# Kernel optimization log

Hardware: AMD Instinct MI355X
Metric: run time of the kernel (lower is better)

The kernel has to match this reference:

```python
import jax, jax.numpy as jnp
import numpy as np

N = 128
HID = 512
NUM_IRREPS = 7

_ISO = np.array([
    [1,0,1,0,0,0,0],
    [0,1,0,1,1,0,0],
    [1,0,1,0,0,0,0],
    [0,1,0,1,1,0,0],
    [0,1,0,1,1,0,0],
    [0,0,0,0,0,1,0],
    [0,0,0,0,0,0,1],
], dtype=np.float32)


def setup_inputs() -> dict:
    key = jax.random.key(0)
    k1, k2 = jax.random.split(key)
    x = jax.random.normal(k1, (2, N, N, HID), dtype=jnp.float32)
    # xavier_uniform with relu gain on [num_irreps, num_irreps]
    gain = float(np.sqrt(2.0))
    bound = gain * float(np.sqrt(6.0 / (NUM_IRREPS + NUM_IRREPS)))
    weight = jax.random.uniform(k2, (NUM_IRREPS, NUM_IRREPS), dtype=jnp.float32,
                                minval=-bound, maxval=bound)
    iso_matrix = jnp.asarray(_ISO)
    return {"x": x, "weight": weight, "iso_matrix": iso_matrix}


def _decompose(M):
    # M: [h, n, n] -> [7, h, n, n], isotypic components under S_n conjugation.
    n = M.shape[-1]
    eye = jnp.eye(n, dtype=M.dtype)
    off = 1.0 - eye
    d = jnp.diagonal(M, axis1=-2, axis2=-1)                 # [h, n]
    dbar = jnp.mean(d, axis=-1, keepdims=True)              # [h, 1]
    P1 = dbar[..., None] * eye                              # diag mean (trivial)
    P2 = (d - dbar)[..., None] * eye                        # diag deviation (standard)
    O = M * off                                             # off-diagonal part
    s = jnp.sum(O, axis=(-2, -1)) / (n * (n - 1))           # [h]
    P3 = s[..., None, None] * off                           # offdiag mean (trivial)
    Op = O - P3
    r = jnp.sum(Op, axis=-1)                                # row sums, [h, n]
    c = jnp.sum(Op, axis=-2)                                # col sums, [h, n]
    xr = ((n - 1) * r + c) / (n * (n - 2))
    yc = ((n - 1) * c + r) / (n * (n - 2))
    P4 = xr[..., :, None] * off                             # row standard copy
    P5 = yc[..., None, :] * off                             # col standard copy
    R = Op - P4 - P5                                        # zero diag / row / col sums
    Rt = jnp.swapaxes(R, -1, -2)
    P6 = 0.5 * (R + Rt)                                     # irrep (n-2,2)
    P7 = 0.5 * (R - Rt)                                     # irrep (n-2,1,1)
    return jnp.stack([P1, P2, P3, P4, P5, P6, P7])          # [7, h, n, n]


def reference(x, weight, iso_matrix):
    # x: [2, n, n, hidden] -> transpose(1,3): [2, hidden, n, n]
    xt = jnp.transpose(x, (0, 3, 2, 1))
    A, B = xt[0], xt[1]                                     # [h, n, n]
    params = weight * iso_matrix                            # [7, 7]
    a = _decompose(A)                                       # [7, h, n, n]
    b = _decompose(B)
    # params @ comps, then sum over output irrep axis (fused into one einsum)
    A_out = jnp.einsum('ij,jhmn->hmn', params, a)
    B_out = jnp.einsum('ij,jhmn->hmn', params, b)
    out = jnp.stack([A_out, B_out])                         # [2, h, n, n]
    return jnp.transpose(out, (0, 3, 2, 1))                 # [2, n, n, hidden]
```

## Files before the change

kernel.cpp:

```cpp
#include <hip/hip_runtime.h>
#include <math.h>

#define N 128
#define HID 512
#define NH (N * HID)
#define SNH ((size_t)N * NH)
#define NPAIRS (N * (N + 1) / 2)

#define OFF_SA 0
#define OFF_SB 131072
#define OFF_DG 262144
#define OFF_XR 393216
#define OFF_YC 524288
#define OFF_SV 655360
#define OFF_DB 656384

typedef float vf4 __attribute__((ext_vector_type(4)));
union F4 { vf4 v; float f[4]; };

__global__ __launch_bounds__(512)
void schur_reduce(const float* __restrict__ x,
                  float* __restrict__ Sa, float* __restrict__ Sb,
                  float* __restrict__ Dg) {
    const int blk = blockIdx.x;
    const int s   = blk >> 7;
    const int idx = blk & 127;
    const int tid = threadIdx.x;
    const int ht  = tid & 127;
    const int q   = tid >> 7;
    const int hoff = ht * 4;

    const float* xs   = x + (size_t)s * SNH;
    const float* xrow = xs + (size_t)idx * NH;

    F4 sa; sa.v = (vf4)(0.f);
    for (int a = q; a < N; a += 4) {
        F4 v; v.v = *reinterpret_cast<const vf4*>(xs + (size_t)a * NH + idx * HID + hoff);
        #pragma unroll
        for (int j = 0; j < 4; ++j) sa.f[j] += v.f[j];
    }
    F4 sb; sb.v = (vf4)(0.f);
    for (int b = q; b < N; b += 4) {
        F4 v; v.v = *reinterpret_cast<const vf4*>(xrow + b * HID + hoff);
        #pragma unroll
        for (int j = 0; j < 4; ++j) sb.f[j] += v.f[j];
    }

    __shared__ F4 red[4][128];
    red[q][ht] = sa;
    __syncthreads();
    if (q == 0) {
        F4 t;
        #pragma unroll
        for (int j = 0; j < 4; ++j)
            t.f[j] = red[0][ht].f[j] + red[1][ht].f[j] + red[2][ht].f[j] + red[3][ht].f[j];
        *reinterpret_cast<vf4*>(Sa + ((size_t)s * N + idx) * HID + hoff) = t.v;
    }
    __syncthreads();
    red[q][ht] = sb;
    __syncthreads();
    if (q == 0) {
        F4 t;
        #pragma unroll
        for (int j = 0; j < 4; ++j)
            t.f[j] = red[0][ht].f[j] + red[1][ht].f[j] + red[2][ht].f[j] + red[3][ht].f[j];
        *reinterpret_cast<vf4*>(Sb + ((size_t)s * N + idx) * HID + hoff) = t.v;
        const vf4 dv = *reinterpret_cast<const vf4*>(xrow + idx * HID + hoff);
        *reinterpret_cast<vf4*>(Dg + ((size_t)s * N + idx) * HID + hoff) = dv;
    }
}

__global__ __launch_bounds__(512)
void schur_stats(const float* __restrict__ Sa, const float* __restrict__ Sb,
                 const float* __restrict__ Dg,
                 float* __restrict__ Xr, float* __restrict__ Yc,
                 float* __restrict__ Sv, float* __restrict__ Db) {
    const int blk = blockIdx.x;
    const int s   = blk >> 4;
    const int hc  = blk & 15;
    const int t   = threadIdx.x;
    const int iq  = t >> 5;
    const int hl  = t & 31;
    const int h   = hc * 32 + hl;
    const size_t base = (size_t)s * N * HID;

    float T = 0.f, D = 0.f;
    #pragma unroll
    for (int i = iq; i < N; i += 16) {
        T += Sa[base + (size_t)i * HID + h];
        D += Dg[base + (size_t)i * HID + h];
    }

    __shared__ float redT[16][32];
    __shared__ float redD[16][32];
    __shared__ float shS[32];
    redT[iq][hl] = T;
    redD[iq][hl] = D;
    __syncthreads();
    if (iq == 0) {
        float Tt = 0.f, Dd = 0.f;
        #pragma unroll
        for (int q = 0; q < 16; ++q) { Tt += redT[q][hl]; Dd += redD[q][hl]; }
        const float sh   = (Tt - Dd) * (1.0f / 16256.0f);
        const float dbar = Dd * (1.0f / 128.0f);
        Sv[s * HID + h] = sh;
        Db[s * HID + h] = dbar;
        shS[hl] = sh;
    }
    __syncthreads();

    const float sh    = shS[hl];
    const float k127s = 127.0f * sh;
    const float inv   = 1.0f / 16128.0f;
    #pragma unroll
    for (int i = iq; i < N; i += 16) {
        const size_t o = base + (size_t)i * HID + h;
        const float d = Dg[o];
        const float r = Sa[o] - d - k127s;
        const float c = Sb[o] - d - k127s;
        Xr[o] = (127.0f * r + c) * inv;
        Yc[o] = (127.0f * c + r) * inv;
    }
}

__global__ __launch_bounds__(256)
void schur_out(const float* __restrict__ x, const float* __restrict__ w,
               const float* __restrict__ iso,
               const float* __restrict__ Xr, const float* __restrict__ Yc,
               const float* __restrict__ Sv, const float* __restrict__ Db,
               float* __restrict__ out) {
    const int t  = threadIdx.x;
    const int k  = t >> 7;
    const int ht = t & 127;
    const int hoff = ht * 4;

    float c[7];
    #pragma unroll
    for (int j = 0; j < 7; ++j) {
        float acc = 0.f;
        #pragma unroll
        for (int i = 0; i < 7; ++i) acc += w[i * 7 + j] * iso[i * 7 + j];
        c[j] = acc;
    }
    const float c1 = c[0], c2 = c[1], c3 = c[2], c4 = c[3], c5 = c[4];
    const float al = 0.5f * (c[5] + c[6]);
    const float be = 0.5f * (c[5] - c[6]);

    const int pg0 = blockIdx.x * 8;

    #define TRI_OFF(aa) ((aa) * N - (((aa) * ((aa) - 1)) >> 1))
    #pragma unroll
    for (int it = 0; it < 4; ++it) {
        const int pg = pg0 + it * 2 + k;
        const int s  = (pg >= NPAIRS) ? 1 : 0;
        const int p  = pg - s * NPAIRS;

        int a = (int)((257.0f - sqrtf((float)(66049 - 8 * p))) * 0.5f);
        if (a < 0) a = 0;
        if (a > N - 1) a = N - 1;
        while (a > 0 && TRI_OFF(a) > p) --a;
        while (TRI_OFF(a + 1) <= p) ++a;
        const int b = a + (p - TRI_OFF(a));

        const size_t sbase    = (size_t)s * SNH;
        const size_t statbase = (size_t)s * N * HID;

        if (a == b) {
            F4 v;  v.v  = *reinterpret_cast<const vf4*>(x + sbase + ((size_t)a * N + a) * HID + hoff);
            F4 db; db.v = *reinterpret_cast<const vf4*>(Db + (size_t)s * HID + hoff);
            F4 o;
            #pragma unroll
            for (int j = 0; j < 4; ++j)
                o.f[j] = c1 * db.f[j] + c2 * (v.f[j] - db.f[j]);
            __builtin_nontemporal_store(o.v,
                reinterpret_cast<vf4*>(out + sbase + ((size_t)a * N + a) * HID + hoff));
            continue;
        }

        F4 va;  va.v  = *reinterpret_cast<const vf4*>(x + sbase + ((size_t)a * N + b) * HID + hoff);
        F4 vb;  vb.v  = *reinterpret_cast<const vf4*>(x + sbase + ((size_t)b * N + a) * HID + hoff);
        F4 xra; xra.v = *reinterpret_cast<const vf4*>(Xr + statbase + (size_t)a * HID + hoff);
        F4 xrb; xrb.v = *reinterpret_cast<const vf4*>(Xr + statbase + (size_t)b * HID + hoff);
        F4 yca; yca.v = *reinterpret_cast<const vf4*>(Yc + statbase + (size_t)a * HID + hoff);
        F4 ycb; ycb.v = *reinterpret_cast<const vf4*>(Yc + statbase + (size_t)b * HID + hoff);
        F4 sh;  sh.v  = *reinterpret_cast<const vf4*>(Sv + (size_t)s * HID + hoff);

        F4 oab, oba;
        #pragma unroll
        for (int j = 0; j < 4; ++j) {
            const float U = va.f[j] - sh.f[j] - xrb.f[j] - yca.f[j];
            const float V = vb.f[j] - sh.f[j] - xra.f[j] - ycb.f[j];
            oab.f[j] = c3 * sh.f[j] + c4 * xrb.f[j] + c5 * yca.f[j] + al * U + be * V;
            oba.f[j] = c3 * sh.f[j] + c4 * xra.f[j] + c5 * ycb.f[j] + al * V + be * U;
        }
        __builtin_nontemporal_store(oab.v,
            reinterpret_cast<vf4*>(out + sbase + ((size_t)a * N + b) * HID + hoff));
        __builtin_nontemporal_store(oba.v,
            reinterpret_cast<vf4*>(out + sbase + ((size_t)b * N + a) * HID + hoff));
    }
}

extern "C" void kernel_launch(void* const* d_in, const int* in_sizes, int n_in,
                              void* d_out, int out_size, void* d_ws, size_t ws_size,
                              hipStream_t stream) {
    const float* x   = (const float*)d_in[0];
    const float* w   = (const float*)d_in[1];
    const float* iso = (const float*)d_in[2];
    float* out = (float*)d_out;
    float* ws  = (float*)d_ws;

    float* Sa = ws + OFF_SA;
    float* Sb = ws + OFF_SB;
    float* Dg = ws + OFF_DG;
    float* Xr = ws + OFF_XR;
    float* Yc = ws + OFF_YC;
    float* Sv = ws + OFF_SV;
    float* Db = ws + OFF_DB;

    schur_reduce<<<2 * N, 512, 0, stream>>>(x, Sa, Sb, Dg);
    schur_stats<<<32, 512, 0, stream>>>(Sa, Sb, Dg, Xr, Yc, Sv, Db);
    schur_out<<<(2 * NPAIRS) / 8, 256, 0, stream>>>(x, w, iso, Xr, Yc, Sv, Db, out);
}
```

Measured before the change: 54.58 us.

## Fuse row and column reductions into single tiled pass over x

Replaces the reduce kernel, which read x twice (once for column sums, once for row sums), with a tiled kernel that reads each 8x8 tile of x once. From that single read it produces per-tile row and column partial sums and the diagonal. The stats kernel then sums the 16 partials per index. This halves the main read traffic of the reduction phase, at the cost of larger partial-sum buffers and more work in the low-parallelism stats kernel.

```diff
diff --git a/kernel.cpp b/kernel.cpp
--- a/kernel.cpp
+++ b/kernel.cpp
@@ -7,71 +7,75 @@
 #define SNH ((size_t)N * NH)
 #define NPAIRS (N * (N + 1) / 2)
 
-#define OFF_SA 0
-#define OFF_SB 131072
-#define OFF_DG 262144
-#define OFF_XR 393216
-#define OFF_YC 524288
-#define OFF_SV 655360
-#define OFF_DB 656384
+#define OFF_PSR 0
+#define OFF_PSC 2097152
+#define OFF_DG  4194304
+#define OFF_XR  4325376
+#define OFF_YC  4456448
+#define OFF_SV  4587520
+#define OFF_DB  4588544
 
 typedef float vf4 __attribute__((ext_vector_type(4)));
 union F4 { vf4 v; float f[4]; };
 
 __global__ __launch_bounds__(512)
-void schur_reduce(const float* __restrict__ x,
-                  float* __restrict__ Sa, float* __restrict__ Sb,
-                  float* __restrict__ Dg) {
-    const int blk = blockIdx.x;
-    const int s   = blk >> 7;
-    const int idx = blk & 127;
+void schur_tile(const float* __restrict__ x,
+                float* __restrict__ PSrow, float* __restrict__ PScol,
+                float* __restrict__ Dg) {
+    const int bi = blockIdx.x;
+    const int s  = bi >> 8;
+    const int ar = (bi >> 4) & 15;
+    const int br = bi & 15;
     const int tid = threadIdx.x;
-    const int ht  = tid & 127;
-    const int q   = tid >> 7;
-    const int hoff = ht * 4;
-
-    const float* xs   = x + (size_t)s * SNH;
-    const float* xrow = xs + (size_t)idx * NH;
-
-    F4 sa; sa.v = (vf4)(0.f);
-    for (int a = q; a < N; a += 4) {
-        F4 v; v.v = *reinterpret_cast<const vf4*>(xs + (size_t)a * NH + idx * HID + hoff);
-        #pragma unroll
-        for (int j = 0; j < 4; ++j) sa.f[j] += v.f[j];
-    }
-    F4 sb; sb.v = (vf4)(0.f);
-    for (int b = q; b < N; b += 4) {
-        F4 v; v.v = *reinterpret_cast<const vf4*>(xrow + b * HID + hoff);
-        #pragma unroll
-        for (int j = 0; j < 4; ++j) sb.f[j] += v.f[j];
-    }
-
-    __shared__ F4 red[4][128];
-    red[q][ht] = sa;
+    const int hg  = tid & 127;
+    const int qd  = tid >> 7;
+    const int hoff = hg * 4;
+    const bool diag = (ar == br);
+
+    const float* tbase = x + (size_t)s * SNH + (size_t)(ar * 8) * NH
+                           + (br * 8) * HID + hoff;
+
+    F4 colacc[8];
+    #pragma unroll
+    for (int b = 0; b < 8; ++b) colacc[b].v = (vf4)(0.f);
+
+    __shared__ F4 red[4][8][128];
+
+    #pragma unroll
+    for (int ra = 0; ra < 2; ++ra) {
+        const int al = qd * 2 + ra;
+        const float* rp = tbase + (size_t)al * NH;
+        F4 rowacc; rowacc.v = (vf4)(0.f);
+        F4 dgv;    dgv.v    = (vf4)(0.f);
+        #pragma unroll
+        for (int b = 0; b < 8; ++b) {
+            F4 v; v.v = *reinterpret_cast<const vf4*>(rp + b * HID);
+            rowacc.v += v.v;
+            colacc[b].v += v.v;
+            if (diag && b == al) dgv = v;
+        }
+        const int a = ar * 8 + al;
+        *reinterpret_cast<vf4*>(PSrow + (((size_t)(s * 16 + br) * 128 + a) * 512 + hoff)) = rowacc.v;
+        if (diag)
+            *reinterpret_cast<vf4*>(Dg + (((size_t)s * 128 + a) * 512 + hoff)) = dgv.v;
+    }
+
+    #pragma unroll
+    for (int b = 0; b < 8; ++b) red[qd][b][hg] = colacc[b];
     __syncthreads();
-    if (q == 0) {
+
+    #pragma unroll
+    for (int k = 0; k < 2; ++k) {
+        const int b = qd * 2 + k;
         F4 t;
-        #pragma unroll
-        for (int j = 0; j < 4; ++j)
-            t.f[j] = red[0][ht].f[j] + red[1][ht].f[j] + red[2][ht].f[j] + red[3][ht].f[j];
-        *reinterpret_cast<vf4*>(Sa + ((size_t)s * N + idx) * HID + hoff) = t.v;
-    }
-    __syncthreads();
-    red[q][ht] = sb;
-    __syncthreads();
-    if (q == 0) {
-        F4 t;
-        #pragma unroll
-        for (int j = 0; j < 4; ++j)
-            t.f[j] = red[0][ht].f[j] + red[1][ht].f[j] + red[2][ht].f[j] + red[3][ht].f[j];
-        *reinterpret_cast<vf4*>(Sb + ((size_t)s * N + idx) * HID + hoff) = t.v;
-        const vf4 dv = *reinterpret_cast<const vf4*>(xrow + idx * HID + hoff);
-        *reinterpret_cast<vf4*>(Dg + ((size_t)s * N + idx) * HID + hoff) = dv;
+        t.v = (red[0][b][hg].v + red[1][b][hg].v) + (red[2][b][hg].v + red[3][b][hg].v);
+        const int gb = br * 8 + b;
+        *reinterpret_cast<vf4*>(PScol + (((size_t)(s * 16 + ar) * 128 + gb) * 512 + hoff)) = t.v;
     }
 }
 
 __global__ __launch_bounds__(512)
-void schur_stats(const float* __restrict__ Sa, const float* __restrict__ Sb,
+void schur_stats(const float* __restrict__ PSrow, const float* __restrict__ PScol,
                  const float* __restrict__ Dg,
                  float* __restrict__ Xr, float* __restrict__ Yc,
                  float* __restrict__ Sv, float* __restrict__ Db) {
@@ -82,13 +86,21 @@
     const int iq  = t >> 5;
     const int hl  = t & 31;
     const int h   = hc * 32 + hl;
-    const size_t base = (size_t)s * N * HID;
-
+
+    float sa8[8], sb8[8], d8[8];
     float T = 0.f, D = 0.f;
     #pragma unroll
-    for (int i = iq; i < N; i += 16) {
-        T += Sa[base + (size_t)i * HID + h];
-        D += Dg[base + (size_t)i * HID + h];
+    for (int k = 0; k < 8; ++k) {
+        const int i = iq + k * 16;
+        float sa = 0.f, sb = 0.f;
+        #pragma unroll
+        for (int tt = 0; tt < 16; ++tt) {
+            sa += PScol[((size_t)(s * 16 + tt) * 128 + i) * 512 + h];
+            sb += PSrow[((size_t)(s * 16 + tt) * 128 + i) * 512 + h];
+        }
+        const float d = Dg[((size_t)s * 128 + i) * 512 + h];
+        sa8[k] = sa; sb8[k] = sb; d8[k] = d;
+        T += sa; D += d;
     }
 
     __shared__ float redT[16][32];
@@ -112,14 +124,15 @@
     const float sh    = shS[hl];
     const float k127s = 127.0f * sh;
     const float inv   = 1.0f / 16128.0f;
-    #pragma unroll
-    for (int i = iq; i < N; i += 16) {
-        const size_t o = base + (size_t)i * HID + h;
-        const float d = Dg[o];
-        const float r = Sa[o] - d - k127s;
-        const float c = Sb[o] - d - k127s;
-        Xr[o] = (127.0f * r + c) * inv;
-        Yc[o] = (127.0f * c + r) * inv;
+    const size_t base = (size_t)s * N * HID;
+    #pragma unroll
+    for (int k = 0; k < 8; ++k) {
+        const int i = iq + k * 16;
+        const float d = d8[k];
+        const float r = sa8[k] - d - k127s;
+        const float c = sb8[k] - d - k127s;
+        Xr[base + (size_t)i * HID + h] = (127.0f * r + c) * inv;
+        Yc[base + (size_t)i * HID + h] = (127.0f * c + r) * inv;
     }
 }
 
@@ -209,15 +222,15 @@
     float* out = (float*)d_out;
     float* ws  = (float*)d_ws;
 
-    float* Sa = ws + OFF_SA;
-    float* Sb = ws + OFF_SB;
-    float* Dg = ws + OFF_DG;
-    float* Xr = ws + OFF_XR;
-    float* Yc = ws + OFF_YC;
-    float* Sv = ws + OFF_SV;
-    float* Db = ws + OFF_DB;
-
-    schur_reduce<<<2 * N, 512, 0, stream>>>(x, Sa, Sb, Dg);
-    schur_stats<<<32, 512, 0, stream>>>(Sa, Sb, Dg, Xr, Yc, Sv, Db);
+    float* PSrow = ws + OFF_PSR;
+    float* PScol = ws + OFF_PSC;
+    float* Dg    = ws + OFF_DG;
+    float* Xr    = ws + OFF_XR;
+    float* Yc    = ws + OFF_YC;
+    float* Sv    = ws + OFF_SV;
+    float* Db    = ws + OFF_DB;
+
+    schur_tile<<<512, 512, 0, stream>>>(x, PSrow, PScol, Dg);
+    schur_stats<<<32, 512, 0, stream>>>(PSrow, PScol, Dg, Xr, Yc, Sv, Db);
     schur_out<<<(2 * NPAIRS) / 8, 256, 0, stream>>>(x, w, iso, Xr, Yc, Sv, Db, out);
 }
```

Result: faster. 52.13 us (-4.5%).
